# Kernel optimization log

Hardware: AMD Instinct MI355X
Metric: run time of the kernel (lower is better)

The kernel has to match this reference:

```python
import jax, jax.numpy as jnp
import numpy as np

# Module hyperparameters (from init_kwargs)
HID = 2048          # hidden_dim
LAT = 512           # kv_latent_dim
H = 16              # num_heads
D = HID // H        # head_dim = 128
FORGET_P = 0.1      # forget_prob
WIN = 128           # window_size
SINK = 16           # persistent_tokens
B, S = 2, 2048
NEG = -1e9


def setup_inputs() -> dict:
    key = jax.random.key(0)
    ks = jax.random.split(key, 8)
    scale = 0.02
    x = jax.random.normal(ks[0], (B, S, HID), dtype=jnp.float32)
    W_q = jax.random.normal(ks[1], (HID, HID), dtype=jnp.float32) * scale
    W_dkv = jax.random.normal(ks[2], (HID, LAT), dtype=jnp.float32) * scale
    W_uk = jax.random.normal(ks[3], (LAT, HID), dtype=jnp.float32) * scale
    W_uv = jax.random.normal(ks[4], (LAT, HID), dtype=jnp.float32) * scale
    W_o = jax.random.normal(ks[5], (HID, HID), dtype=jnp.float32) * scale
    # Bernoulli(forget_prob) per-key forget mask (1 = forget this token)
    forget_mask = jax.random.bernoulli(ks[6], FORGET_P, (B, S)).astype(jnp.int32)
    return {"x": x, "W_q": W_q, "W_dkv": W_dkv, "W_uk": W_uk,
            "W_uv": W_uv, "W_o": W_o, "forget_mask": forget_mask, "top_k": 64}


def reference(x, W_q, W_dkv, W_uk, W_uv, W_o, forget_mask, top_k):
    Bx, Sx, _ = x.shape
    # Queries; keys/values via shared compressed KV latent (MLA-style)
    q = (x @ W_q).reshape(Bx, Sx, H, D)
    c = x @ W_dkv                                   # [B, S, LAT]
    k = (c @ W_uk).reshape(Bx, Sx, H, D)
    v = (c @ W_uv).reshape(Bx, Sx, H, D)

    scores = jnp.einsum('bqhd,bkhd->bhqk', q, k) / np.float32(np.sqrt(D))

    qi = jnp.arange(Sx)[:, None]
    ki = jnp.arange(Sx)[None, :]
    causal = ki <= qi
    local = ki >= qi - (WIN - 1)
    sink = ki < SINK                  # persistent sink tokens always visible
    allow = causal & (local | sink)   # [S, S]

    # Forgetting: drop non-sink, non-self keys flagged by the forget mask
    forget = (forget_mask[:, None, None, :] == 1) \
             & (ki >= SINK)[None, None] & (ki != qi)[None, None]   # [B,1,S,S]
    keep = allow[None, None] & ~forget

    s = jnp.where(keep, scores, jnp.asarray(NEG, scores.dtype))
    # Top-k selection per query: keep only the k largest scores
    kth = jax.lax.top_k(s, top_k)[0][..., -1:]
    s = jnp.where(s >= kth, s, jnp.asarray(NEG, s.dtype))

    attn = jax.nn.softmax(s, axis=-1)
    out = jnp.einsum('bhqk,bkhd->bqhd', attn, v).reshape(Bx, Sx, HID)
    return out @ W_o
```

## Files before the change

kernel.cpp:

```cpp
#include <hip/hip_runtime.h>
#include <hip/hip_bf16.h>

typedef unsigned short u16;
typedef unsigned int u32;
typedef unsigned long long u64;
typedef __bf16 bf16x8 __attribute__((ext_vector_type(8)));
typedef float f32x4 __attribute__((ext_vector_type(4)));
typedef u16 u16x4 __attribute__((ext_vector_type(4)));
typedef u16 u16x8 __attribute__((ext_vector_type(8)));

static constexpr int BB = 2, SS = 2048, HIDC = 2048, LATC = 512, NH = 16, HD = 128;
static constexpr int MROWS = BB * SS;
static constexpr float NEGV = -1e9f;

__device__ __forceinline__ u16 f2bf(float f) {
  __hip_bfloat16 h = __float2bfloat16(f);
  return __builtin_bit_cast(u16, h);
}
__device__ __forceinline__ float bf2f(u16 u) {
  return __uint_as_float(((u32)u) << 16);
}
__device__ __forceinline__ void load_lds16(const void* g, void* l) {
  __builtin_amdgcn_global_load_lds(
      (const __attribute__((address_space(1))) void*)g,
      (__attribute__((address_space(3))) void*)l, 16, 0, 0);
}
__device__ __forceinline__ void xcd_remap(int& bx, int& by) {
  const int nbx = gridDim.x;
  const int nb = nbx * gridDim.y;
  int lin = blockIdx.x + nbx * blockIdx.y;
  lin = (lin & 7) * (nb >> 3) + (lin >> 3);
  bx = lin % nbx;
  by = lin / nbx;
}

template <int MODE>
__global__ __launch_bounds__(256, 2) void gemm_bt(
    const u16* __restrict__ A, const u16* __restrict__ Bt,
    float* __restrict__ C, u16* __restrict__ Cb, int M, int N, int K,
    size_t sA, size_t sB, size_t sC) {
  __shared__ u16 As[128 * 64];
  __shared__ u16 Bs[128 * 64];
  const int tid = threadIdx.x;
  const int lane = tid & 63;
  const int wv = tid >> 6;
  const int wr = wv >> 1, wc = wv & 1;
  int bx, by;
  xcd_remap(bx, by);
  const int m0 = bx * 128, n0 = by * 128;
  A += sA * blockIdx.z;
  Bt += sB * blockIdx.z;
  if constexpr (MODE == 0) C += sC * blockIdx.z;
  if constexpr (MODE == 2) Cb += sC * blockIdx.z;

  f32x4 acc[4][4];
#pragma unroll
  for (int i = 0; i < 4; ++i)
#pragma unroll
    for (int j = 0; j < 4; ++j) acc[i][j] = (f32x4){0.f, 0.f, 0.f, 0.f};

  int srow[4], sgc[4];
#pragma unroll
  for (int j = 0; j < 4; ++j) {
    int e = j * 2048 + tid * 8;
    int row = e >> 6;
    int slot = (e >> 3) & 7;
    srow[j] = row;
    sgc[j] = (slot ^ (row & 7)) * 8;
  }

  for (int k0 = 0; k0 < K; k0 += 64) {
    __syncthreads();
#pragma unroll
    for (int j = 0; j < 4; ++j) {
      const u16* ga = A + (size_t)(m0 + srow[j]) * K + k0 + sgc[j];
      const u16* gb = Bt + (size_t)(n0 + srow[j]) * K + k0 + sgc[j];
      load_lds16(ga, &As[j * 2048 + wv * 512]);
      load_lds16(gb, &Bs[j * 2048 + wv * 512]);
    }
    asm volatile("s_waitcnt vmcnt(0)" ::: "memory");
    __syncthreads();

#pragma unroll
    for (int kk = 0; kk < 2; ++kk) {
      bf16x8 afr[4], bfr[4];
      const int kg = kk * 4 + (lane >> 4);
#pragma unroll
      for (int i = 0; i < 4; ++i) {
        int ar = wr * 64 + i * 16 + (lane & 15);
        afr[i] = *(const bf16x8*)&As[ar * 64 + ((kg ^ (ar & 7)) << 3)];
        int br = wc * 64 + i * 16 + (lane & 15);
        bfr[i] = *(const bf16x8*)&Bs[br * 64 + ((kg ^ (br & 7)) << 3)];
      }
#pragma unroll
      for (int mi = 0; mi < 4; ++mi)
#pragma unroll
        for (int ni = 0; ni < 4; ++ni)
          acc[mi][ni] = __builtin_amdgcn_mfma_f32_16x16x32_bf16(
              afr[mi], bfr[ni], acc[mi][ni], 0, 0, 0);
    }
  }

#pragma unroll
  for (int mi = 0; mi < 4; ++mi) {
#pragma unroll
    for (int ni = 0; ni < 4; ++ni) {
      const int row = m0 + wr * 64 + mi * 16 + (lane >> 4) * 4;
      const int col = n0 + wc * 64 + ni * 16 + (lane & 15);
#pragma unroll
      for (int r = 0; r < 4; ++r) {
        size_t off = (size_t)(row + r) * N + col;
        if constexpr (MODE == 0) C[off] = acc[mi][ni][r];
        if constexpr (MODE == 2) Cb[off] = f2bf(acc[mi][ni][r]);
      }
    }
  }
}

template <int TN, int MODE>
__global__ __launch_bounds__(256, 2) void gemm_split_bt(
    const u16* __restrict__ Ah, const u16* __restrict__ Al,
    const u16* __restrict__ Bth, const u16* __restrict__ Btl,
    float* __restrict__ C, u16* __restrict__ Ch, u16* __restrict__ Cl,
    int M, int N, int K) {
  constexpr int NI = TN / 32;
  __shared__ u16 Ash[128 * 64];
  __shared__ u16 Asl[128 * 64];
  __shared__ u16 Bsh[TN * 64];
  __shared__ u16 Bsl[TN * 64];
  const int tid = threadIdx.x;
  const int lane = tid & 63;
  const int wv = tid >> 6;
  const int wr = wv >> 1, wc = wv & 1;
  const int l15 = lane & 15, lhi = lane >> 4;
  int bx, by;
  xcd_remap(bx, by);
  const int m0 = bx * 128, n0 = by * TN;

  f32x4 acc[4][NI];
#pragma unroll
  for (int i = 0; i < 4; ++i)
#pragma unroll
    for (int j = 0; j < NI; ++j) acc[i][j] = (f32x4){0.f, 0.f, 0.f, 0.f};

  int srow[4], sgc[4];
#pragma unroll
  for (int j = 0; j < 4; ++j) {
    int e = j * 2048 + tid * 8;
    int row = e >> 6;
    int slot = (e >> 3) & 7;
    srow[j] = row;
    sgc[j] = (slot ^ (row & 7)) * 8;
  }

  for (int k0 = 0; k0 < K; k0 += 64) {
    __syncthreads();
#pragma unroll
    for (int j = 0; j < 4; ++j) {
      const size_t ao = (size_t)(m0 + srow[j]) * K + k0 + sgc[j];
      load_lds16(Ah + ao, &Ash[j * 2048 + wv * 512]);
      load_lds16(Al + ao, &Asl[j * 2048 + wv * 512]);
    }
#pragma unroll
    for (int j = 0; j < NI; ++j) {
      const size_t bo = (size_t)(n0 + srow[j]) * K + k0 + sgc[j];
      load_lds16(Bth + bo, &Bsh[j * 2048 + wv * 512]);
      load_lds16(Btl + bo, &Bsl[j * 2048 + wv * 512]);
    }
    asm volatile("s_waitcnt vmcnt(0)" ::: "memory");
    __syncthreads();

#pragma unroll
    for (int kk = 0; kk < 2; ++kk) {
      const int kg = kk * 4 + lhi;
      bf16x8 afh[4], afl[4], bfh[NI], bfl[NI];
#pragma unroll
      for (int i = 0; i < 4; ++i) {
        const int ar = wr * 64 + i * 16 + l15;
        const int off = ar * 64 + ((kg ^ (ar & 7)) << 3);
        afh[i] = *(const bf16x8*)&Ash[off];
        afl[i] = *(const bf16x8*)&Asl[off];
      }
#pragma unroll
      for (int i = 0; i < NI; ++i) {
        const int br = wc * (TN / 2) + i * 16 + l15;
        const int off = br * 64 + ((kg ^ (br & 7)) << 3);
        bfh[i] = *(const bf16x8*)&Bsh[off];
        bfl[i] = *(const bf16x8*)&Bsl[off];
      }
#pragma unroll
      for (int mi = 0; mi < 4; ++mi)
#pragma unroll
        for (int ni = 0; ni < NI; ++ni) {
          acc[mi][ni] = __builtin_amdgcn_mfma_f32_16x16x32_bf16(
              afh[mi], bfh[ni], acc[mi][ni], 0, 0, 0);
          acc[mi][ni] = __builtin_amdgcn_mfma_f32_16x16x32_bf16(
              afh[mi], bfl[ni], acc[mi][ni], 0, 0, 0);
          acc[mi][ni] = __builtin_amdgcn_mfma_f32_16x16x32_bf16(
              afl[mi], bfh[ni], acc[mi][ni], 0, 0, 0);
        }
    }
  }

#pragma unroll
  for (int mi = 0; mi < 4; ++mi) {
#pragma unroll
    for (int ni = 0; ni < NI; ++ni) {
      const int row = m0 + wr * 64 + mi * 16 + lhi * 4;
      const int col = n0 + wc * (TN / 2) + ni * 16 + l15;
#pragma unroll
      for (int r = 0; r < 4; ++r) {
        const size_t off = (size_t)(row + r) * N + col;
        const float v = acc[mi][ni][r];
        if constexpr (MODE == 0) C[off] = v;
        if constexpr (MODE == 3) {
          const u16 hh = f2bf(v);
          Ch[off] = hh;
          Cl[off] = f2bf(v - bf2f(hh));
        }
      }
    }
  }
}

__global__ __launch_bounds__(256) void prep_all(
    const float* __restrict__ x, u16* __restrict__ xh, u16* __restrict__ xl,
    const float* __restrict__ Wq, u16* __restrict__ Wqh, u16* __restrict__ Wql,
    const float* __restrict__ Wdkv, u16* __restrict__ Wdh, u16* __restrict__ Wdl,
    const float* __restrict__ Wuk, u16* __restrict__ Wukh, u16* __restrict__ Wukl,
    const float* __restrict__ Wuv, u16* __restrict__ Wuvt,
    const float* __restrict__ Wo, u16* __restrict__ Wot) {
  const int bx = blockIdx.x, tid = threadIdx.x;
  if (bx < 8192) {
    const size_t i = ((size_t)bx * 256 + tid) * 4;
    f32x4 v = *(const f32x4*)(x + i);
    u16x4 hh, ll;
#pragma unroll
    for (int e = 0; e < 4; ++e) {
      const u16 hi = f2bf(v[e]);
      hh[e] = hi;
      ll[e] = f2bf(v[e] - bf2f(hi));
    }
    *(u16x4*)(xh + i) = hh;
    *(u16x4*)(xl + i) = ll;
    return;
  }
  __shared__ float t[32][33];
  const float* W;
  u16 *Th, *Tl = nullptr;
  int K, N, gx, gy;
  if (bx < 12288) {
    const int q = bx - 8192;
    W = Wq; Th = Wqh; Tl = Wql; K = 2048; N = 2048; gx = q & 63; gy = q >> 6;
  } else if (bx < 13312) {
    const int q = bx - 12288;
    W = Wdkv; Th = Wdh; Tl = Wdl; K = 2048; N = 512; gx = q & 15; gy = q >> 4;
  } else if (bx < 14336) {
    const int q = bx - 13312;
    W = Wuk; Th = Wukh; Tl = Wukl; K = 512; N = 2048; gx = q & 63; gy = q >> 6;
  } else if (bx < 15360) {
    const int q = bx - 14336;
    W = Wuv; Th = Wuvt; K = 512; N = 2048; gx = q & 63; gy = q >> 6;
  } else {
    const int q = bx - 15360;
    W = Wo; Th = Wot; K = 2048; N = 2048; gx = q & 63; gy = q >> 6;
  }
  const int tx = tid & 31, ty0 = tid >> 5;
#pragma unroll
  for (int i = 0; i < 4; ++i) {
    const int ty = ty0 + i * 8;
    t[ty][tx] = W[(size_t)(gy * 32 + ty) * N + gx * 32 + tx];
  }
  __syncthreads();
#pragma unroll
  for (int i = 0; i < 4; ++i) {
    const int ty = ty0 + i * 8;
    const float v = t[tx][ty];
    const size_t o = (size_t)(gx * 32 + ty) * K + gy * 32 + tx;
    const u16 hi = f2bf(v);
    Th[o] = hi;
    if (Tl) Tl[o] = f2bf(v - bf2f(hi));
  }
}

__device__ __forceinline__ u32 fmap(float f) {
  u32 b = __float_as_uint(f);
  return (b & 0x80000000u) ? ~b : (b | 0x80000000u);
}
__device__ __forceinline__ float unfmap(u32 u) {
  return (u & 0x80000000u) ? __uint_as_float(u ^ 0x80000000u)
                           : __uint_as_float(~u);
}

__global__ __launch_bounds__(512, 2) void attn_v6(
    const u16* __restrict__ qbh, const u16* __restrict__ qbl,
    const u16* __restrict__ khi, const u16* __restrict__ klo,
    const u16* __restrict__ vt, const int* __restrict__ forget,
    const int* __restrict__ topk, u16* __restrict__ ab) {
  __shared__ u16 KP[2 * 64 * 128];
  __shared__ float St[64 * 68];
  __shared__ u16 Vb1[64 * 128];
  __shared__ int fm[256];
  u16* const Kh = KP;
  u16* const Kl = KP + 64 * 128;
  u16* const Pb = KP;
  u16* const Vt0 = (u16*)St;

  const float scale = 0.08838834764831845f;
  const int tid = threadIdx.x, lane = tid & 63, wv = tid >> 6;
  const int lin = blockIdx.x + 32 * (blockIdx.y + 16 * blockIdx.z);
  const int nl = (lin & 7) * 128 + (lin >> 3);
  const int q0 = (nl & 31) * 64;
  const int h = (nl >> 5) & 15;
  const int b = nl >> 9;
  const int mt = wv >> 1, nh = wv & 1;
  const int l15 = lane & 15, lhi = lane >> 4;
  const int nt = (q0 >= 256) ? 4 : (q0 / 64 + 1);
  const int KTOP = topk[0];

  auto kbase = [&](int t) {
    return (q0 >= 256) ? (t == 0 ? 0 : q0 + t * 64 - 192) : t * 64;
  };
  auto stage_k = [&](int t) {
    const int kbt = kbase(t);
#pragma unroll
    for (int p = 0; p < 2; ++p) {
      const int c = p * 512 + tid;
      const int row = c >> 4, sl = c & 15;
      const size_t src = (size_t)(b * SS + kbt + row) * HIDC + h * HD +
                         ((sl ^ (row & 7)) << 3);
      load_lds16(khi + src, Kh + (p * 512 + wv * 64) * 8);
      load_lds16(klo + src, Kl + (p * 512 + wv * 64) * 8);
    }
  };
  auto stage_vt = [&](int t, u16* dst) {
    const int kbt = kbase(t);
#pragma unroll
    for (int p = 0; p < 2; ++p) {
      const int c = p * 512 + tid;
      const int d = c >> 3, sl = c & 7;
      const u16* src = vt + ((size_t)(b * HIDC + h * HD + d)) * SS + kbt +
                       ((sl ^ (d & 7)) << 3);
      load_lds16(src, dst + (p * 512 + wv * 64) * 8);
    }
  };

  if (tid < 256)
    fm[tid] = ((tid >> 6) < nt) ? forget[b * SS + kbase(tid >> 6) + (tid & 63)] : 0;

  u32 koff[4][2];
#pragma unroll
  for (int kt = 0; kt < 4; ++kt)
#pragma unroll
    for (int ni = 0; ni < 2; ++ni) {
      const int key = nh * 32 + ni * 16 + l15;
      const int kg = kt * 4 + lhi;
      koff[kt][ni] = key * 128 + ((kg ^ (key & 7)) << 3);
    }
  const int arow = mt * 16 + l15;
  u32 pboff[2];
#pragma unroll
  for (int ks = 0; ks < 2; ++ks)
    pboff[ks] = arow * 256 + (((ks * 4 + lhi) ^ (arow & 7)) << 3);
  u32 voff[2][4];
#pragma unroll
  for (int ks = 0; ks < 2; ++ks)
#pragma unroll
    for (int t2 = 0; t2 < 4; ++t2) {
      const int drow = nh * 64 + t2 * 16 + l15;
      voff[ks][t2] = drow * 64 + (((ks * 4 + lhi) ^ (drow & 7)) << 3);
    }
  const u32 stw = (u32)(mt * 16 + lhi * 4) * 68 + nh * 32 + l15;

  u16x8 ah[4], al[4];
  const size_t qrow = (size_t)(b * SS + q0 + mt * 16 + l15) * HIDC + h * HD;
#pragma unroll
  for (int kt = 0; kt < 4; ++kt) {
    ah[kt] = *(const u16x8*)(qbh + qrow + kt * 32 + lhi * 8);
    al[kt] = *(const u16x8*)(qbl + qrow + kt * 32 + lhi * 8);
  }

  u32 uu[8][4];
#pragma unroll
  for (int i = 0; i < 8; ++i)
#pragma unroll
    for (int j = 0; j < 4; ++j) uu[i][j] = 0u;

  stage_k(0);
#pragma unroll
  for (int t = 0; t < 4; ++t) {
    if (t < nt) {
      asm volatile("s_waitcnt vmcnt(0)" ::: "memory");
      __syncthreads();

      f32x4 acc0 = (f32x4){0.f, 0.f, 0.f, 0.f};
      f32x4 acc1 = (f32x4){0.f, 0.f, 0.f, 0.f};
#pragma unroll
      for (int kt = 0; kt < 4; ++kt) {
#pragma unroll
        for (int ni = 0; ni < 2; ++ni) {
          const bf16x8 bh = *(const bf16x8*)(Kh + koff[kt][ni]);
          const bf16x8 bl = *(const bf16x8*)(Kl + koff[kt][ni]);
          f32x4 a = ni ? acc1 : acc0;
          a = __builtin_amdgcn_mfma_f32_16x16x32_bf16(
              __builtin_bit_cast(bf16x8, ah[kt]), bh, a, 0, 0, 0);
          a = __builtin_amdgcn_mfma_f32_16x16x32_bf16(
              __builtin_bit_cast(bf16x8, ah[kt]), bl, a, 0, 0, 0);
          a = __builtin_amdgcn_mfma_f32_16x16x32_bf16(
              __builtin_bit_cast(bf16x8, al[kt]), bh, a, 0, 0, 0);
          if (ni) acc1 = a; else acc0 = a;
        }
      }
#pragma unroll
      for (int ni = 0; ni < 2; ++ni)
#pragma unroll
        for (int r = 0; r < 4; ++r)
          St[stw + r * 68 + ni * 16] = (ni ? acc1 : acc0)[r] * scale;
      __syncthreads();

      if (t + 1 < nt) stage_k(t + 1);

      const int kbt = kbase(t);
      const int key = kbt + lane;
      const bool fok = !(fm[t * 64 + lane] != 0 && key >= 16);
      const bool sk = key < 16;
#pragma unroll
      for (int i = 0; i < 8; ++i) {
        const int qi = q0 + wv * 8 + i;
        const bool valid =
            key <= qi && (key >= qi - 127 || sk) && (fok || key == qi);
        uu[i][t] = fmap(valid ? St[(wv * 8 + i) * 68 + lane] : NEGV);
      }
    }
  }
  __syncthreads();

  stage_vt(0, Vt0);

  u32 tl[8], th[8];
#pragma unroll
  for (int i = 0; i < 8; ++i) { tl[i] = 0u; th[i] = 0xFFFFFFFFu; }
  for (int it = 0; it < 32; ++it) {
    bool any = false;
#pragma unroll
    for (int i = 0; i < 8; ++i) {
      if (tl[i] < th[i]) {
        any = true;
        const u32 mid = tl[i] + ((th[i] - tl[i]) >> 1) + 1u;
        const int cnt = __popcll(__ballot(uu[i][0] >= mid)) +
                        __popcll(__ballot(uu[i][1] >= mid)) +
                        __popcll(__ballot(uu[i][2] >= mid)) +
                        __popcll(__ballot(uu[i][3] >= mid));
        if (cnt == KTOP) {
          tl[i] = mid;
          th[i] = mid;
        } else if (cnt > KTOP) {
          tl[i] = mid;
        } else {
          th[i] = mid - 1u;
        }
      }
    }
    if (!any) break;
  }

#pragma unroll
  for (int i = 0; i < 8; ++i) {
    const int r = wv * 8 + i;
    float sv[4], m = NEGV;
#pragma unroll
    for (int j = 0; j < 4; ++j) {
      sv[j] = unfmap(uu[i][j]);
      m = (uu[i][j] >= tl[i]) ? fmaxf(m, sv[j]) : m;
    }
#pragma unroll
    for (int off = 32; off > 0; off >>= 1) m = fmaxf(m, __shfl_xor(m, off));
    float e[4], z = 0.f;
#pragma unroll
    for (int j = 0; j < 4; ++j) {
      e[j] = (uu[i][j] >= tl[i]) ? __expf(sv[j] - m) : 0.f;
      z += e[j];
    }
#pragma unroll
    for (int off = 32; off > 0; off >>= 1) z += __shfl_xor(z, off);
    const float rz = 1.f / z;
#pragma unroll
    for (int j = 0; j < 4; ++j) {
      const int c = lane + 64 * j;
      const int sl = c >> 3;
      Pb[r * 256 + ((sl ^ (r & 7)) << 3) + (c & 7)] = f2bf(e[j] * rz);
    }
  }

  asm volatile("s_waitcnt vmcnt(0)" ::: "memory");
  __syncthreads();

  f32x4 pacc[4];
#pragma unroll
  for (int t2 = 0; t2 < 4; ++t2) pacc[t2] = (f32x4){0.f, 0.f, 0.f, 0.f};

#pragma unroll
  for (int t = 0; t < 4; ++t) {
    if (t < nt) {
      if (t + 1 < nt) stage_vt(t + 1, ((t + 1) & 1) ? Vb1 : Vt0);
      const u16* Vcur = (t & 1) ? Vb1 : Vt0;
#pragma unroll
      for (int ks = 0; ks < 2; ++ks) {
        const bf16x8 af = *(const bf16x8*)(Pb + pboff[ks] + t * 64);
#pragma unroll
        for (int t2 = 0; t2 < 4; ++t2) {
          const bf16x8 bf_ = *(const bf16x8*)(Vcur + voff[ks][t2]);
          pacc[t2] = __builtin_amdgcn_mfma_f32_16x16x32_bf16(af, bf_, pacc[t2],
                                                             0, 0, 0);
        }
      }
      if (t + 1 < nt) {
        asm volatile("s_waitcnt vmcnt(0)" ::: "memory");
        __syncthreads();
      }
    }
  }

#pragma unroll
  for (int t2 = 0; t2 < 4; ++t2)
#pragma unroll
    for (int r = 0; r < 4; ++r) {
      const int row = q0 + mt * 16 + lhi * 4 + r;
      const int col = h * HD + nh * 64 + t2 * 16 + l15;
      ab[(size_t)(b * SS + row) * HIDC + col] = f2bf(pacc[t2][r]);
    }
}

extern "C" void kernel_launch(void* const* d_in, const int* in_sizes, int n_in,
                              void* d_out, int out_size, void* d_ws, size_t ws_size,
                              hipStream_t stream) {
  const float* x = (const float*)d_in[0];
  const float* W_q = (const float*)d_in[1];
  const float* W_dkv = (const float*)d_in[2];
  const float* W_uk = (const float*)d_in[3];
  const float* W_uv = (const float*)d_in[4];
  const float* W_o = (const float*)d_in[5];
  const int* forget = (const int*)d_in[6];
  const int* topk = (const int*)d_in[7];
  float* out = (float*)d_out;

  char* p = (char*)d_ws;
  auto take = [&](size_t n) {
    char* r = p;
    p += (n + 255) & ~(size_t)255;
    return r;
  };

  u16* xb_hi = (u16*)take((size_t)MROWS * HIDC * 2);
  u16* xb_lo = (u16*)take((size_t)MROWS * HIDC * 2);
  u16* Wqh = (u16*)take((size_t)HIDC * HIDC * 2);
  u16* Wql = (u16*)take((size_t)HIDC * HIDC * 2);
  u16* Wdh = (u16*)take((size_t)LATC * HIDC * 2);
  u16* Wdl = (u16*)take((size_t)LATC * HIDC * 2);
  u16* Wukh = (u16*)take((size_t)HIDC * LATC * 2);
  u16* Wukl = (u16*)take((size_t)HIDC * LATC * 2);
  u16* Wuvt = (u16*)take((size_t)HIDC * LATC * 2);
  u16* Wot = (u16*)take((size_t)HIDC * HIDC * 2);
  u16* qbh = (u16*)take((size_t)MROWS * HIDC * 2);
  u16* qbl = (u16*)take((size_t)MROWS * HIDC * 2);
  u16* cbh = (u16*)take((size_t)MROWS * LATC * 2);
  u16* cbl = (u16*)take((size_t)MROWS * LATC * 2);
  u16* vt = (u16*)take((size_t)BB * HIDC * SS * 2);
  u16* khi = xb_hi;
  u16* klo = xb_lo;
  u16* ab = Wqh;

  prep_all<<<dim3(19456), dim3(256), 0, stream>>>(
      x, xb_hi, xb_lo, W_q, Wqh, Wql, W_dkv, Wdh, Wdl, W_uk, Wukh, Wukl,
      W_uv, Wuvt, W_o, Wot);

  gemm_split_bt<128, 3><<<dim3(MROWS / 128, HIDC / 128), 256, 0, stream>>>(
      xb_hi, xb_lo, Wqh, Wql, nullptr, qbh, qbl, MROWS, HIDC, HIDC);
  gemm_split_bt<64, 3><<<dim3(MROWS / 128, LATC / 64), 256, 0, stream>>>(
      xb_hi, xb_lo, Wdh, Wdl, nullptr, cbh, cbl, MROWS, LATC, HIDC);
  gemm_split_bt<128, 3><<<dim3(MROWS / 128, HIDC / 128), 256, 0, stream>>>(
      cbh, cbl, Wukh, Wukl, nullptr, khi, klo, MROWS, HIDC, LATC);
  gemm_bt<2><<<dim3(HIDC / 128, SS / 128, BB), 256, 0, stream>>>(
      Wuvt, cbh, nullptr, vt, HIDC, SS, LATC,
      0, (size_t)SS * LATC, (size_t)HIDC * SS);
  attn_v6<<<dim3(SS / 64, NH, BB), dim3(512), 0, stream>>>(
      qbh, qbl, khi, klo, vt, forget, topk, ab);
  gemm_bt<0><<<dim3(MROWS / 128, HIDC / 128), 256, 0, stream>>>(
      ab, Wot, out, nullptr, MROWS, HIDC, HIDC, 0, 0, 0);
}
```

Before: 327.8 us.

## Prefetch V tiles earlier in attention and drop XCD block remapping in GEMMs

The attention kernel now starts loading the first V tile into a dedicated LDS buffer at the same time as the first K tile. The second V tile is loaded during the top-k search, and the PV loop becomes a two-ahead pipeline with partial vmcnt waits, so V loads overlap with score computation and selection instead of stalling the PV phase. Separately, the GEMM kernels stop remapping block indices across XCDs and use plain blockIdx order, which changes L2 locality. Vb1 must not alias anything still live during the score phase, and the counted vmcnt waits must match how many loads are actually outstanding.

```diff
diff --git a/kernel.cpp b/kernel.cpp
--- a/kernel.cpp
+++ b/kernel.cpp
@@ -24,14 +24,6 @@
   __builtin_amdgcn_global_load_lds(
       (const __attribute__((address_space(1))) void*)g,
       (__attribute__((address_space(3))) void*)l, 16, 0, 0);
-}
-__device__ __forceinline__ void xcd_remap(int& bx, int& by) {
-  const int nbx = gridDim.x;
-  const int nb = nbx * gridDim.y;
-  int lin = blockIdx.x + nbx * blockIdx.y;
-  lin = (lin & 7) * (nb >> 3) + (lin >> 3);
-  bx = lin % nbx;
-  by = lin / nbx;
 }
 
 template <int MODE>
@@ -45,9 +37,7 @@
   const int lane = tid & 63;
   const int wv = tid >> 6;
   const int wr = wv >> 1, wc = wv & 1;
-  int bx, by;
-  xcd_remap(bx, by);
-  const int m0 = bx * 128, n0 = by * 128;
+  const int m0 = blockIdx.x * 128, n0 = blockIdx.y * 128;
   A += sA * blockIdx.z;
   Bt += sB * blockIdx.z;
   if constexpr (MODE == 0) C += sC * blockIdx.z;
@@ -133,9 +123,7 @@
   const int wv = tid >> 6;
   const int wr = wv >> 1, wc = wv & 1;
   const int l15 = lane & 15, lhi = lane >> 4;
-  int bx, by;
-  xcd_remap(bx, by);
-  const int m0 = bx * 128, n0 = by * TN;
+  const int m0 = blockIdx.x * 128, n0 = blockIdx.y * TN;
 
   f32x4 acc[4][NI];
 #pragma unroll
@@ -292,7 +280,7 @@
                            : __uint_as_float(~u);
 }
 
-__global__ __launch_bounds__(512, 2) void attn_v6(
+__global__ __launch_bounds__(512, 2) void attn_v7(
     const u16* __restrict__ qbh, const u16* __restrict__ qbl,
     const u16* __restrict__ khi, const u16* __restrict__ klo,
     const u16* __restrict__ vt, const int* __restrict__ forget,
@@ -387,6 +375,8 @@
     for (int j = 0; j < 4; ++j) uu[i][j] = 0u;
 
   stage_k(0);
+  stage_vt(0, Vb1);
+
 #pragma unroll
   for (int t = 0; t < 4; ++t) {
     if (t < nt) {
@@ -435,7 +425,7 @@
   }
   __syncthreads();
 
-  stage_vt(0, Vt0);
+  if (nt > 1) stage_vt(1, Vt0);
 
   u32 tl[8], th[8];
 #pragma unroll
@@ -502,8 +492,16 @@
 #pragma unroll
   for (int t = 0; t < 4; ++t) {
     if (t < nt) {
-      if (t + 1 < nt) stage_vt(t + 1, ((t + 1) & 1) ? Vb1 : Vt0);
-      const u16* Vcur = (t & 1) ? Vb1 : Vt0;
+      if (t == 2) {
+        if (nt > 3) asm volatile("s_waitcnt vmcnt(2)" ::: "memory");
+        else asm volatile("s_waitcnt vmcnt(0)" ::: "memory");
+        __syncthreads();
+      }
+      if (t == 3) {
+        asm volatile("s_waitcnt vmcnt(0)" ::: "memory");
+        __syncthreads();
+      }
+      u16* const Vcur = (t & 1) ? Vt0 : Vb1;
 #pragma unroll
       for (int ks = 0; ks < 2; ++ks) {
         const bf16x8 af = *(const bf16x8*)(Pb + pboff[ks] + t * 64);
@@ -514,9 +512,9 @@
                                                              0, 0, 0);
         }
       }
-      if (t + 1 < nt) {
-        asm volatile("s_waitcnt vmcnt(0)" ::: "memory");
+      if (t + 2 < nt) {
         __syncthreads();
+        stage_vt(t + 2, Vcur);
       }
     }
   }
@@ -583,7 +581,7 @@
   gemm_bt<2><<<dim3(HIDC / 128, SS / 128, BB), 256, 0, stream>>>(
       Wuvt, cbh, nullptr, vt, HIDC, SS, LATC,
       0, (size_t)SS * LATC, (size_t)HIDC * SS);
-  attn_v6<<<dim3(SS / 64, NH, BB), dim3(512), 0, stream>>>(
+  attn_v7<<<dim3(SS / 64, NH, BB), dim3(512), 0, stream>>>(
       qbh, qbl, khi, klo, vt, forget, topk, ab);
   gemm_bt<0><<<dim3(MROWS / 128, HIDC / 128), 256, 0, stream>>>(
       ab, Wot, out, nullptr, MROWS, HIDC, HIDC, 0, 0, 0);
```

Measured after the change: 308.1 us. -6.0%, faster.
